# Kernel tuning notes

Hardware: AMD Instinct MI355X
Metric: run time of the kernel (lower is better)

Reference implementation:

```python
import jax, jax.numpy as jnp
import numpy as np

B, R, K, S = 512, 264, 32, 9
SUB_ENDS = np.array([28, 58, 92, 121, 150, 180, 210, 240, 264], dtype=np.int32)


def setup_inputs() -> dict:
    key = jax.random.key(0)
    embeddings = jax.random.normal(key, (B, R, K), dtype=jnp.float32)
    return {"embeddings": embeddings, "subnetwork_ends": jnp.asarray(SUB_ENDS)}


def reference(embeddings, subnetwork_ends):
    # subnetwork_ends are static structural constants (cumulative block ends).
    ends = np.asarray(jax.device_get(subnetwork_ends))
    starts = np.concatenate([np.zeros(1, dtype=ends.dtype), ends[:-1]])
    sizes = ends - starts                      # [S]
    n_sub = ends.shape[0]
    seg = np.repeat(np.arange(n_sub), sizes)   # [R] segment id per ROI

    # adjacency: batched gram matrix, [B, R, R]
    adjacency = jnp.einsum('brk,bpk->brp', embeddings, embeddings)

    # intra-network adjacency: zero out cross-block entries
    intra_mask = jnp.asarray(seg[:, None] == seg[None, :])  # [R, R] bool
    intra = adjacency * intra_mask                          # [B, R, R]

    # inter-network matrix: block means via one fused segment reduce
    # (replaces the O(S^2) per-block slice+mean loop in the original)
    one_hot = jnp.asarray(np.eye(n_sub, dtype=np.float32)[seg])          # [R, S]
    counts = jnp.asarray((sizes[:, None] * sizes[None, :]).astype(np.float32))  # [S, S]
    inter = jnp.einsum('brp,rs,pt->bst', adjacency, one_hot, one_hot) / counts  # [B, S, S]

    return intra[..., None], inter[..., None], adjacency[..., None]
```

## Files before the change

### kernel.cpp

```cpp
#include <hip/hip_runtime.h>


constexpr int B_ = 512, R_ = 264, K_ = 32, S_ = 9;
constexpr int LDR_ = 40;
constexpr long long NI_ = (long long)B_ * R_ * R_;
constexpr long long NS_ = (long long)B_ * S_ * S_;

typedef float f32x4 __attribute__((ext_vector_type(4)));
typedef float vf4 __attribute__((ext_vector_type(4)));
typedef short bf16x8 __attribute__((ext_vector_type(8)));

static __device__ inline unsigned short f2bf(float f) {
  unsigned int u = __builtin_bit_cast(unsigned int, f);
  u += 0x7fffu + ((u >> 16) & 1u);
  return (unsigned short)(u >> 16);
}

__global__ __launch_bounds__(512, 8) void adj_intra_mfma(
    const float* __restrict__ emb, float* __restrict__ out) {
  __shared__ unsigned short Ebf[272 * LDR_];
  __shared__ unsigned char seg_lut[272];

  const int b = blockIdx.x;
  const int stripe = blockIdx.y;
  const int tid = threadIdx.x;
  const float* __restrict__ eb = emb + (size_t)b * R_ * K_;

  for (int idx = tid; idx < (R_ * K_) / 4; idx += 512) {
    const int r = idx >> 3;
    const int k4 = (idx & 7) * 4;
    const f32x4 v = *reinterpret_cast<const f32x4*>(eb + r * K_ + k4);
    const unsigned int lo = (unsigned int)f2bf(v.x) | ((unsigned int)f2bf(v.y) << 16);
    const unsigned int hi = (unsigned int)f2bf(v.z) | ((unsigned int)f2bf(v.w) << 16);
    uint2 pk; pk.x = lo; pk.y = hi;
    *reinterpret_cast<uint2*>(&Ebf[r * LDR_ + k4]) = pk;
  }
  if (tid < 8 * LDR_) Ebf[264 * LDR_ + tid] = 0;
  if (tid < 272) {
    const int x = tid;
    seg_lut[x] = (x >= 28) + (x >= 58) + (x >= 92) + (x >= 121) +
                 (x >= 150) + (x >= 180) + (x >= 210) + (x >= 240);
  }
  __syncthreads();

  const int wave = tid >> 6, lane = tid & 63;
  const int half = lane >> 4;
  const int l15 = lane & 15;

  const int ntiles = (stripe < 4) ? 4 * 17 : 17;
  float* __restrict__ intra_out = out;
  float* __restrict__ adj_out = out + NI_ + NS_;
  const size_t bbase = (size_t)b * ((long long)R_ * R_);

  for (int t = wave; t < ntiles; t += 8) {
    const int tr = stripe * 4 + t / 17;
    const int tc = t % 17;
    const bf16x8 af = *reinterpret_cast<const bf16x8*>(
        &Ebf[(tr * 16 + l15) * LDR_ + half * 8]);
    const bf16x8 bfr = *reinterpret_cast<const bf16x8*>(
        &Ebf[(tc * 16 + l15) * LDR_ + half * 8]);
    f32x4 acc = {0.f, 0.f, 0.f, 0.f};
    acc = __builtin_amdgcn_mfma_f32_16x16x32_bf16(af, bfr, acc, 0, 0, 0);

    const int j = tc * 16 + l15;
    if (j < R_) {
      const int sj = seg_lut[j];
      const int ibase = tr * 16 + half * 4;
      const size_t obase = bbase + (size_t)ibase * R_ + j;
#pragma unroll
      for (int q = 0; q < 4; ++q) {
        const int i = ibase + q;
        if (i < R_) {
          const float v = acc[q];
          const int si = seg_lut[i];
          adj_out[obase + (size_t)q * R_] = v;
          intra_out[obase + (size_t)q * R_] = (si == sj) ? v : 0.0f;
        }
      }
    }
  }
}

__global__ __launch_bounds__(256) void inter_k(
    const float* __restrict__ emb, float* __restrict__ out) {
  constexpr int ENDS[S_] = {28, 58, 92, 121, 150, 180, 210, 240, 264};
  constexpr int STARTS[S_] = {0, 28, 58, 92, 121, 150, 180, 210, 240};
  constexpr float SZ[S_] = {28.f, 30.f, 34.f, 29.f, 29.f, 30.f, 30.f, 30.f, 24.f};

  __shared__ float ps[S_ * 8 * 32];
  __shared__ float ss[32 * 12];

  const int b = blockIdx.x, tid = threadIdx.x;
  const int k = tid & 31, q = tid >> 5;
  const float* __restrict__ eb = emb + (size_t)b * R_ * K_;

#pragma unroll
  for (int s = 0; s < S_; ++s) {
    const int lo = STARTS[s], len = ENDS[s] - STARTS[s];
    const int c0 = lo + (len * q) / 8, c1 = lo + (len * (q + 1)) / 8;
    float a = 0.0f;
    for (int r = c0; r < c1; ++r) a += eb[r * K_ + k];
    ps[(s * 8 + q) * 32 + k] = a;
  }
  __syncthreads();
  for (int c = tid; c < S_ * 32; c += 256) {
    const int s = c >> 5, kk = c & 31;
    float a = 0.0f;
#pragma unroll
    for (int qq = 0; qq < 8; ++qq) a += ps[(s * 8 + qq) * 32 + kk];
    ss[kk * 12 + s] = a;
  }
  __syncthreads();
  if (tid < S_ * S_) {
    const int s = tid / S_, t = tid % S_;
    float d = 0.0f;
    for (int kk = 0; kk < 32; ++kk) d += ss[kk * 12 + s] * ss[kk * 12 + t];
    d /= (SZ[s] * SZ[t]);
    out[NI_ + (size_t)b * (S_ * S_) + tid] = d;
  }
}

extern "C" void kernel_launch(void* const* d_in, const int* in_sizes, int n_in,
                              void* d_out, int out_size, void* d_ws,
                              size_t ws_size, hipStream_t stream) {
  const float* emb = (const float*)d_in[0];
  float* out = (float*)d_out;
  hipLaunchKernelGGL(adj_intra_mfma, dim3(B_, 5), dim3(512), 0, stream, emb, out);
  hipLaunchKernelGGL(inter_k, dim3(B_), dim3(256), 0, stream, emb, out);
}
```

Measured before the change: 356.2 us.

## Process all row stripes per batch in one block, reusing LDS-staged embeddings

Collapses the 5-stripe grid into one block per batch. Each block now converts the embeddings to bf16 in LDS once instead of five times, and each wave keeps its A fragment and row segment ids in registers while it sweeps all 17 column tiles. The result is 5x fewer blocks and less redundant global loading and conversion. In exchange, grid parallelism drops to 512 blocks, and the leftover 16th row tile leaves some waves idle.

```diff
diff --git a/kernel.cpp b/kernel.cpp
--- a/kernel.cpp
+++ b/kernel.cpp
@@ -7,7 +7,6 @@
 constexpr long long NS_ = (long long)B_ * S_ * S_;
 
 typedef float f32x4 __attribute__((ext_vector_type(4)));
-typedef float vf4 __attribute__((ext_vector_type(4)));
 typedef short bf16x8 __attribute__((ext_vector_type(8)));
 
 static __device__ inline unsigned short f2bf(float f) {
@@ -22,7 +21,6 @@
   __shared__ unsigned char seg_lut[272];
 
   const int b = blockIdx.x;
-  const int stripe = blockIdx.y;
   const int tid = threadIdx.x;
   const float* __restrict__ eb = emb + (size_t)b * R_ * K_;
 
@@ -30,9 +28,9 @@
     const int r = idx >> 3;
     const int k4 = (idx & 7) * 4;
     const f32x4 v = *reinterpret_cast<const f32x4*>(eb + r * K_ + k4);
-    const unsigned int lo = (unsigned int)f2bf(v.x) | ((unsigned int)f2bf(v.y) << 16);
-    const unsigned int hi = (unsigned int)f2bf(v.z) | ((unsigned int)f2bf(v.w) << 16);
-    uint2 pk; pk.x = lo; pk.y = hi;
+    uint2 pk;
+    pk.x = (unsigned int)f2bf(v.x) | ((unsigned int)f2bf(v.y) << 16);
+    pk.y = (unsigned int)f2bf(v.z) | ((unsigned int)f2bf(v.w) << 16);
     *reinterpret_cast<uint2*>(&Ebf[r * LDR_ + k4]) = pk;
   }
   if (tid < 8 * LDR_) Ebf[264 * LDR_ + tid] = 0;
@@ -47,34 +45,64 @@
   const int half = lane >> 4;
   const int l15 = lane & 15;
 
-  const int ntiles = (stripe < 4) ? 4 * 17 : 17;
   float* __restrict__ intra_out = out;
   float* __restrict__ adj_out = out + NI_ + NS_;
   const size_t bbase = (size_t)b * ((long long)R_ * R_);
 
-  for (int t = wave; t < ntiles; t += 8) {
-    const int tr = stripe * 4 + t / 17;
-    const int tc = t % 17;
+
+#pragma unroll
+  for (int rr = 0; rr < 2; ++rr) {
+    const int tr = wave + rr * 8;
     const bf16x8 af = *reinterpret_cast<const bf16x8*>(
         &Ebf[(tr * 16 + l15) * LDR_ + half * 8]);
-    const bf16x8 bfr = *reinterpret_cast<const bf16x8*>(
-        &Ebf[(tc * 16 + l15) * LDR_ + half * 8]);
-    f32x4 acc = {0.f, 0.f, 0.f, 0.f};
-    acc = __builtin_amdgcn_mfma_f32_16x16x32_bf16(af, bfr, acc, 0, 0, 0);
+    const int ibase = tr * 16 + half * 4;
+    const int si0 = seg_lut[ibase + 0], si1 = seg_lut[ibase + 1];
+    const int si2 = seg_lut[ibase + 2], si3 = seg_lut[ibase + 3];
+    float* __restrict__ adj_row = adj_out + bbase + (size_t)ibase * R_;
+    float* __restrict__ intra_row = intra_out + bbase + (size_t)ibase * R_;
 
-    const int j = tc * 16 + l15;
-    if (j < R_) {
-      const int sj = seg_lut[j];
-      const int ibase = tr * 16 + half * 4;
-      const size_t obase = bbase + (size_t)ibase * R_ + j;
+    for (int tc = 0; tc < 17; ++tc) {
+      const bf16x8 bfr = *reinterpret_cast<const bf16x8*>(
+          &Ebf[(tc * 16 + l15) * LDR_ + half * 8]);
+      f32x4 acc = {0.f, 0.f, 0.f, 0.f};
+      acc = __builtin_amdgcn_mfma_f32_16x16x32_bf16(af, bfr, acc, 0, 0, 0);
+      const int j = tc * 16 + l15;
+      if (j < R_) {
+        const int sj = seg_lut[j];
+        adj_row[(size_t)0 * R_ + j] = acc[0];
+        adj_row[(size_t)1 * R_ + j] = acc[1];
+        adj_row[(size_t)2 * R_ + j] = acc[2];
+        adj_row[(size_t)3 * R_ + j] = acc[3];
+        intra_row[(size_t)0 * R_ + j] = (si0 == sj) ? acc[0] : 0.0f;
+        intra_row[(size_t)1 * R_ + j] = (si1 == sj) ? acc[1] : 0.0f;
+        intra_row[(size_t)2 * R_ + j] = (si2 == sj) ? acc[2] : 0.0f;
+        intra_row[(size_t)3 * R_ + j] = (si3 == sj) ? acc[3] : 0.0f;
+      }
+    }
+  }
+
+  {
+    const int tr = 16;
+    const bf16x8 af = *reinterpret_cast<const bf16x8*>(
+        &Ebf[(tr * 16 + l15) * LDR_ + half * 8]);
+    const int ibase = tr * 16 + half * 4;
+    for (int tc = wave; tc < 17; tc += 8) {
+      const bf16x8 bfr = *reinterpret_cast<const bf16x8*>(
+          &Ebf[(tc * 16 + l15) * LDR_ + half * 8]);
+      f32x4 acc = {0.f, 0.f, 0.f, 0.f};
+      acc = __builtin_amdgcn_mfma_f32_16x16x32_bf16(af, bfr, acc, 0, 0, 0);
+      const int j = tc * 16 + l15;
+      if (j < R_) {
+        const int sj = seg_lut[j];
 #pragma unroll
-      for (int q = 0; q < 4; ++q) {
-        const int i = ibase + q;
-        if (i < R_) {
-          const float v = acc[q];
-          const int si = seg_lut[i];
-          adj_out[obase + (size_t)q * R_] = v;
-          intra_out[obase + (size_t)q * R_] = (si == sj) ? v : 0.0f;
+        for (int q = 0; q < 4; ++q) {
+          const int i = ibase + q;
+          if (i < R_) {
+            const float v = acc[q];
+            const size_t idx = bbase + (size_t)i * R_ + j;
+            adj_out[idx] = v;
+            intra_out[idx] = (seg_lut[i] == sj) ? v : 0.0f;
+          }
         }
       }
     }
@@ -125,6 +153,6 @@
                               size_t ws_size, hipStream_t stream) {
   const float* emb = (const float*)d_in[0];
   float* out = (float*)d_out;
-  hipLaunchKernelGGL(adj_intra_mfma, dim3(B_, 5), dim3(512), 0, stream, emb, out);
+  hipLaunchKernelGGL(adj_intra_mfma, dim3(B_), dim3(512), 0, stream, emb, out);
   hipLaunchKernelGGL(inter_k, dim3(B_), dim3(256), 0, stream, emb, out);
 }
```

Measured after the change: 393.4 us. +10.4%, slower.

## Assign half tile-rows per wave and cut per-batch blocks from five to two

Applied to the files above, without the earlier changes.

The grid changes from five stripes per batch to two, so each batch's embedding is loaded and converted to bf16 into shared memory only twice instead of five times. Each wave now owns half of a 16-row tile row. It loads the A fragment once and loops over 8 or 9 column tiles, reusing the A fragment and the row segment ids across iterations. The cost is fewer, larger blocks. With 17 half-rows per block spread over 8 waves, one wave does an extra iteration, so load across waves is uneven. Output store patterns are unchanged.

```diff
diff --git a/kernel.cpp b/kernel.cpp
--- a/kernel.cpp
+++ b/kernel.cpp
@@ -7,7 +7,6 @@
 constexpr long long NS_ = (long long)B_ * S_ * S_;
 
 typedef float f32x4 __attribute__((ext_vector_type(4)));
-typedef float vf4 __attribute__((ext_vector_type(4)));
 typedef short bf16x8 __attribute__((ext_vector_type(8)));
 
 static __device__ inline unsigned short f2bf(float f) {
@@ -30,9 +29,9 @@
     const int r = idx >> 3;
     const int k4 = (idx & 7) * 4;
     const f32x4 v = *reinterpret_cast<const f32x4*>(eb + r * K_ + k4);
-    const unsigned int lo = (unsigned int)f2bf(v.x) | ((unsigned int)f2bf(v.y) << 16);
-    const unsigned int hi = (unsigned int)f2bf(v.z) | ((unsigned int)f2bf(v.w) << 16);
-    uint2 pk; pk.x = lo; pk.y = hi;
+    uint2 pk;
+    pk.x = (unsigned int)f2bf(v.x) | ((unsigned int)f2bf(v.y) << 16);
+    pk.y = (unsigned int)f2bf(v.z) | ((unsigned int)f2bf(v.w) << 16);
     *reinterpret_cast<uint2*>(&Ebf[r * LDR_ + k4]) = pk;
   }
   if (tid < 8 * LDR_) Ebf[264 * LDR_ + tid] = 0;
@@ -47,35 +46,40 @@
   const int half = lane >> 4;
   const int l15 = lane & 15;
 
-  const int ntiles = (stripe < 4) ? 4 * 17 : 17;
   float* __restrict__ intra_out = out;
   float* __restrict__ adj_out = out + NI_ + NS_;
   const size_t bbase = (size_t)b * ((long long)R_ * R_);
 
-  for (int t = wave; t < ntiles; t += 8) {
-    const int tr = stripe * 4 + t / 17;
-    const int tc = t % 17;
+  for (int j = stripe * 17 + wave; j < stripe * 17 + 17; j += 8) {
+    const int tr = j >> 1;
+    const int th = j & 1;
     const bf16x8 af = *reinterpret_cast<const bf16x8*>(
         &Ebf[(tr * 16 + l15) * LDR_ + half * 8]);
-    const bf16x8 bfr = *reinterpret_cast<const bf16x8*>(
-        &Ebf[(tc * 16 + l15) * LDR_ + half * 8]);
-    f32x4 acc = {0.f, 0.f, 0.f, 0.f};
-    acc = __builtin_amdgcn_mfma_f32_16x16x32_bf16(af, bfr, acc, 0, 0, 0);
+    const int ibase = tr * 16 + half * 4;
+    const bool rowok = (ibase + 3) < R_;
+    const int si0 = seg_lut[ibase + 0], si1 = seg_lut[ibase + 1];
+    const int si2 = seg_lut[ibase + 2], si3 = seg_lut[ibase + 3];
+    float* __restrict__ adj_row = adj_out + bbase + (size_t)ibase * R_;
+    float* __restrict__ intra_row = intra_out + bbase + (size_t)ibase * R_;
 
-    const int j = tc * 16 + l15;
-    if (j < R_) {
-      const int sj = seg_lut[j];
-      const int ibase = tr * 16 + half * 4;
-      const size_t obase = bbase + (size_t)ibase * R_ + j;
-#pragma unroll
-      for (int q = 0; q < 4; ++q) {
-        const int i = ibase + q;
-        if (i < R_) {
-          const float v = acc[q];
-          const int si = seg_lut[i];
-          adj_out[obase + (size_t)q * R_] = v;
-          intra_out[obase + (size_t)q * R_] = (si == sj) ? v : 0.0f;
-        }
+    const int tc_lo = th ? 9 : 0;
+    const int tc_hi = th ? 17 : 9;
+    for (int tc = tc_lo; tc < tc_hi; ++tc) {
+      const bf16x8 bfr = *reinterpret_cast<const bf16x8*>(
+          &Ebf[(tc * 16 + l15) * LDR_ + half * 8]);
+      f32x4 acc = {0.f, 0.f, 0.f, 0.f};
+      acc = __builtin_amdgcn_mfma_f32_16x16x32_bf16(af, bfr, acc, 0, 0, 0);
+      const int col = tc * 16 + l15;
+      if (rowok && col < R_) {
+        const int sj = seg_lut[col];
+        adj_row[(size_t)0 * R_ + col] = acc[0];
+        adj_row[(size_t)1 * R_ + col] = acc[1];
+        adj_row[(size_t)2 * R_ + col] = acc[2];
+        adj_row[(size_t)3 * R_ + col] = acc[3];
+        intra_row[(size_t)0 * R_ + col] = (si0 == sj) ? acc[0] : 0.0f;
+        intra_row[(size_t)1 * R_ + col] = (si1 == sj) ? acc[1] : 0.0f;
+        intra_row[(size_t)2 * R_ + col] = (si2 == sj) ? acc[2] : 0.0f;
+        intra_row[(size_t)3 * R_ + col] = (si3 == sj) ? acc[3] : 0.0f;
       }
     }
   }
@@ -125,6 +129,6 @@
                               size_t ws_size, hipStream_t stream) {
   const float* emb = (const float*)d_in[0];
   float* out = (float*)d_out;
-  hipLaunchKernelGGL(adj_intra_mfma, dim3(B_, 5), dim3(512), 0, stream, emb, out);
+  hipLaunchKernelGGL(adj_intra_mfma, dim3(B_, 2), dim3(512), 0, stream, emb, out);
   hipLaunchKernelGGL(inter_k, dim3(B_), dim3(256), 0, stream, emb, out);
 }
```

After: 373.5 us. 4.8% more time.
